# Optimization experiments

Measured on AMD Instinct MI355X. Metric: run time of the kernel, lower is better.

Reference implementation:

```python
import jax, jax.numpy as jnp
import numpy as np

B, T, D, H = 2, 2048, 1024, 16
DK = D // H


def setup_inputs() -> dict:
    key = jax.random.key(0)
    ks = jax.random.split(key, 12)
    s = 0.02
    return {
        "query": jax.random.normal(ks[0], (B, T, D), jnp.float32),
        "key": jax.random.normal(ks[1], (B, T, D), jnp.float32),
        "value": jax.random.normal(ks[2], (B, T, D), jnp.float32),
        "mask": jax.random.randint(ks[3], (B, T), 0, 2) != 0,  # True = keep
        "Wq": jax.random.normal(ks[4], (D, D), jnp.float32) * s,
        "bq": jnp.zeros((D,), jnp.float32),
        "Wk": jax.random.normal(ks[5], (D, D), jnp.float32) * s,
        "bk": jnp.zeros((D,), jnp.float32),
        "Wv": jax.random.normal(ks[6], (D, D), jnp.float32) * s,
        "bv": jnp.zeros((D,), jnp.float32),
        "Wo": jax.random.normal(ks[7], (D, D), jnp.float32) * s,
        "bo": jnp.zeros((D,), jnp.float32),
    }


def _split_heads(x):
    # [B, S, D] -> [B, H, S, DK]
    b, s, _ = x.shape
    return x.reshape(b, s, H, DK).transpose(0, 2, 1, 3)


def reference(query, key, value, mask, Wq, bq, Wk, bk, Wv, bv, Wo, bo):
    # torch Linear: y = x @ W.T + b
    q = _split_heads(query @ Wq.T + bq)   # [B,H,T,DK]
    k = _split_heads(key @ Wk.T + bk)     # [B,H,S,DK]
    v = _split_heads(value @ Wv.T + bv)   # [B,H,S,DK]
    scale = 1.0 / np.sqrt(DK).astype(np.float32)
    scores = jnp.einsum('bhtd,bhsd->bhts', q, k) * scale  # [B,H,T,S]
    # key-padding mask [B,S] -> broadcast [B,1,1,S], True = keep
    scores = jnp.where(mask[:, None, None, :], scores, -jnp.inf)
    attn = jax.nn.softmax(scores, axis=-1)
    out = jnp.einsum('bhts,bhsd->bhtd', attn, v)           # [B,H,T,DK]
    out = out.transpose(0, 2, 1, 3).reshape(query.shape[0], -1, D)
    return out @ Wo.T + bo
```

## Files before the change

kernel.cpp:

```cpp
#include <hip/hip_runtime.h>
#include <stdint.h>

#define B_SZ 2
#define T_SEQ 2048
#define DMODEL 1024
#define NHEAD 16
#define DKH 64
#define M_ROWS (B_SZ * T_SEQ)

#define LDT 72

#define INP_E  4194304u
#define W_E    1048576u

typedef __bf16 bf16x8 __attribute__((ext_vector_type(8)));
typedef float  f32x4  __attribute__((ext_vector_type(4)));

__device__ __forceinline__ unsigned short f2bf(float f) {
    unsigned u = __builtin_bit_cast(unsigned, f);
    u += 0x7fffu + ((u >> 16) & 1u);
    return (unsigned short)(u >> 16);
}
__device__ __forceinline__ uint4 cvt8(const float* p) {
    float4 f0 = *(const float4*)p, f1 = *(const float4*)(p + 4);
    uint4 r;
    r.x = (unsigned)f2bf(f0.x) | ((unsigned)f2bf(f0.y) << 16);
    r.y = (unsigned)f2bf(f0.z) | ((unsigned)f2bf(f0.w) << 16);
    r.z = (unsigned)f2bf(f1.x) | ((unsigned)f2bf(f1.y) << 16);
    r.w = (unsigned)f2bf(f1.z) | ((unsigned)f2bf(f1.w) << 16);
    return r;
}

__device__ __forceinline__ void async16(const unsigned short* g, unsigned short* l) {
    __builtin_amdgcn_global_load_lds(
        (const __attribute__((address_space(1))) void*)g,
        (__attribute__((address_space(3))) void*)l, 16, 0, 0);
}

__global__ __launch_bounds__(256) void cvt_all(
    const float* __restrict__ q, const float* __restrict__ k, const float* __restrict__ v,
    const float* __restrict__ wq, const float* __restrict__ wk,
    const float* __restrict__ wv, const float* __restrict__ wo,
    unsigned short* __restrict__ wsb)
{
    int blk = blockIdx.x;
    const float* src; unsigned short* dst; int lb;
    if      (blk < 2048) { src = q;  dst = wsb;                       lb = blk; }
    else if (blk < 4096) { src = k;  dst = wsb + INP_E;               lb = blk - 2048; }
    else if (blk < 6144) { src = v;  dst = wsb + 2 * INP_E;           lb = blk - 4096; }
    else if (blk < 6656) { src = wq; dst = wsb + 3 * INP_E;           lb = blk - 6144; }
    else if (blk < 7168) { src = wk; dst = wsb + 3 * INP_E + W_E;     lb = blk - 6656; }
    else if (blk < 7680) { src = wv; dst = wsb + 3 * INP_E + 2 * W_E; lb = blk - 7168; }
    else                 { src = wo; dst = wsb + 3 * INP_E + 3 * W_E; lb = blk - 7680; }
    size_t i = ((size_t)lb * 256 + threadIdx.x) * 8;
    *(uint4*)&dst[i] = cvt8(src + i);
}

template<int C_MODE, int MT>
__device__ __forceinline__ void gemm_core(
    const unsigned short* __restrict__ A, const unsigned short* __restrict__ W,
    const float* __restrict__ bias, void* __restrict__ C,
    int N, int K, int bx, int by,
    unsigned short* sA, unsigned short* sB)
{
    const int tid  = threadIdx.x;
    const int wave = tid >> 6, lane = tid & 63;
    const int quad = lane >> 4, l15 = lane & 15;
    const int TM = MT * 32;
    const int m0 = by * TM, n0 = bx * 128;
    const int wm = (wave & 1) * (MT * 16), wn = (wave >> 1) * 64;

    f32x4 acc[MT][4] = {};

    for (int k0 = 0; k0 < K; k0 += 64) {
        __syncthreads();
        #pragma unroll
        for (int i = 0; i < MT; i++) {
            int c   = tid + 256 * i;
            int row = c >> 3;
            int gk  = ((c & 7) ^ (row & 7)) * 8;
            int sb  = (wave * 64 + 256 * i) * 8;
            async16(&A[(size_t)(m0 + row) * K + k0 + gk], sA + sb);
        }
        #pragma unroll
        for (int i = 0; i < 4; i++) {
            int c   = tid + 256 * i;
            int row = c >> 3;
            int gk  = ((c & 7) ^ (row & 7)) * 8;
            int sb  = (wave * 64 + 256 * i) * 8;
            async16(&W[(size_t)(n0 + row) * K + k0 + gk], sB + sb);
        }
        __syncthreads();
        const int sw = l15 & 7;
        #pragma unroll
        for (int ks = 0; ks < 2; ks++) {
            bf16x8 af[MT], bfv[4];
            #pragma unroll
            for (int mt = 0; mt < MT; mt++)
                af[mt] = *(const bf16x8*)&sA[(wm + mt * 16 + l15) * 64 +
                                             (((ks * 4 + quad) ^ sw) * 8)];
            #pragma unroll
            for (int nt = 0; nt < 4; nt++)
                bfv[nt] = *(const bf16x8*)&sB[(wn + nt * 16 + l15) * 64 +
                                              (((ks * 4 + quad) ^ sw) * 8)];
            #pragma unroll
            for (int mt = 0; mt < MT; mt++)
                #pragma unroll
                for (int nt = 0; nt < 4; nt++)
                    acc[mt][nt] = __builtin_amdgcn_mfma_f32_16x16x32_bf16(
                        af[mt], bfv[nt], acc[mt][nt], 0, 0, 0);
        }
    }

    if (C_MODE == 2) {
        #pragma unroll
        for (int mt = 0; mt < MT; mt++) {
            #pragma unroll
            for (int r = 0; r < 4; r++) {
                int m = m0 + wm + mt * 16 + quad * 4 + r;
                float bm = bias[m];
                #pragma unroll
                for (int nt = 0; nt < 4; nt++) {
                    int n = n0 + wn + nt * 16 + l15;
                    int bb = n >> 11, t = n & 2047;
                    ((unsigned short*)C)[((size_t)bb * 1024 + m) * 2048 + t] =
                        f2bf(acc[mt][nt][r] + bm);
                }
            }
        }
    } else {
        #pragma unroll
        for (int nt = 0; nt < 4; nt++) {
            int n = n0 + wn + nt * 16 + l15;
            float bv = bias[n];
            #pragma unroll
            for (int mt = 0; mt < MT; mt++) {
                #pragma unroll
                for (int r = 0; r < 4; r++) {
                    int m = m0 + wm + mt * 16 + quad * 4 + r;
                    float val = acc[mt][nt][r] + bv;
                    if (C_MODE == 1) ((float*)C)[(size_t)m * N + n] = val;
                    else ((unsigned short*)C)[(size_t)m * N + n] = f2bf(val);
                }
            }
        }
    }
}

__global__ __launch_bounds__(256) void gemm_qkv(
    const unsigned short* __restrict__ Qb, const unsigned short* __restrict__ Kb,
    const unsigned short* __restrict__ Vb,
    const unsigned short* __restrict__ Wqb, const unsigned short* __restrict__ Wkb,
    const unsigned short* __restrict__ Wvb,
    const float* __restrict__ bq, const float* __restrict__ bk, const float* __restrict__ bv,
    unsigned short* __restrict__ Qp, unsigned short* __restrict__ Kp,
    unsigned short* __restrict__ Vt)
{
    __shared__ __align__(16) unsigned short sA[128 * 64];
    __shared__ __align__(16) unsigned short sB[128 * 64];
    const int z = blockIdx.z, id = blockIdx.x;
    if (z < 2) {
        gemm_core<0, 4>(z ? Kb : Qb, z ? Wkb : Wqb, z ? bk : bq, z ? Kp : Qp,
                        DMODEL, DMODEL, id & 7, id >> 3, sA, sB);
    } else {
        gemm_core<2, 4>(Wvb, Vb, bv, Vt, M_ROWS, DMODEL, id & 31, id >> 5, sA, sB);
    }
}

__global__ __launch_bounds__(256) void gemm_o(
    const unsigned short* __restrict__ AO, const unsigned short* __restrict__ Wob,
    const float* __restrict__ bo, float* __restrict__ out)
{
    __shared__ __align__(16) unsigned short sA[64 * 64];
    __shared__ __align__(16) unsigned short sB[128 * 64];
    const int id = blockIdx.x;
    gemm_core<1, 2>(AO, Wob, bo, out, DMODEL, DMODEL, id & 7, id >> 3, sA, sB);
}

#define QBLK 128
#define KVB 64

__global__ __launch_bounds__(512, 4) void attn_kernel(
    const unsigned short* __restrict__ Qp,
    const unsigned short* __restrict__ Kp,
    const unsigned short* __restrict__ Vt,
    const int* __restrict__ maskp,
    unsigned short* __restrict__ Op)
{
    __shared__ __align__(16) unsigned short sKV[2][2][KVB * 64];
    __shared__ __align__(16) unsigned short sP[8 * 32 * LDT];
    __shared__ float smf[T_SEQ];

    const int tid  = threadIdx.x;
    const int wave = tid >> 6, lane = tid & 63;
    const int g    = wave >> 2, wl = wave & 3;
    const int quad = lane >> 4, l15 = lane & 15;
    const int qblk = blockIdx.x, h = blockIdx.y, b = blockIdx.z;

    const float SCL2 = 0.125f * 1.44269504089f;
    const float MNEG = -30000.f;

    bf16x8 aq[2][2];
    #pragma unroll
    for (int mt = 0; mt < 2; mt++) {
        const int qrow = qblk * QBLK + wl * 32 + mt * 16 + l15;
        const unsigned short* qptr =
            Qp + (size_t)(b * T_SEQ + qrow) * DMODEL + h * DKH + quad * 8;
        aq[mt][0] = *(const bf16x8*)qptr;
        aq[mt][1] = *(const bf16x8*)(qptr + 32);
    }

    const unsigned short* Kb_ = Kp + (size_t)b * T_SEQ * DMODEL + h * DKH;
    const unsigned short* VtB = Vt + ((size_t)b * DMODEL + h * DKH) * T_SEQ;

    f32x4 O[2][4] = {};
    float l_r[2][4] = {};
    unsigned short* sPw = sP + wave * 32 * LDT;

    #pragma unroll
    for (int j = 0; j < 4; j++) {
        int i = tid + 512 * j;
        smf[i] = maskp[b * T_SEQ + i] ? 0.f : MNEG;
    }

    const int sw = l15 & 7;
    for (int rr = 0; rr < T_SEQ / (2 * KVB); ++rr) {
        #pragma unroll
        for (int i = 0; i < 2; i++) {
            int c    = tid + 512 * i;
            int tile = c >> 9, cc = c & 511;
            int row  = cc >> 3;
            int gk   = ((cc & 7) ^ (row & 7)) * 8;
            int sb   = (wave * 64 + 512 * i) * 8;
            int key0 = rr * 128 + tile * 64;
            async16(&Kb_[(size_t)(key0 + row) * DMODEL + gk], &sKV[0][0][0] + sb);
            async16(&VtB[(size_t)row * T_SEQ + key0 + gk], &sKV[1][0][0] + sb);
        }
        __syncthreads();

        const unsigned short* sKp = &sKV[0][g][0];
        const unsigned short* sVp = &sKV[1][g][0];
        const int s0 = (2 * rr + g) * KVB;

        f32x4 S[2][4];
        __builtin_amdgcn_s_setprio(1);
        #pragma unroll
        for (int nt = 0; nt < 4; nt++) {
            const unsigned short* kr = &sKp[(nt * 16 + l15) * 64];
            const bf16x8 kf0 = *(const bf16x8*)&kr[(quad ^ sw) * 8];
            const bf16x8 kf1 = *(const bf16x8*)&kr[((quad + 4) ^ sw) * 8];
            #pragma unroll
            for (int mt = 0; mt < 2; mt++) {
                f32x4 z = {};
                z = __builtin_amdgcn_mfma_f32_16x16x32_bf16(aq[mt][0], kf0, z, 0, 0, 0);
                z = __builtin_amdgcn_mfma_f32_16x16x32_bf16(aq[mt][1], kf1, z, 0, 0, 0);
                S[mt][nt] = z;
            }
        }
        __builtin_amdgcn_s_setprio(0);

        #pragma unroll
        for (int mt = 0; mt < 2; mt++) {
            #pragma unroll
            for (int nt = 0; nt < 4; nt++) {
                float madd = smf[s0 + nt * 16 + l15];
                #pragma unroll
                for (int r = 0; r < 4; r++) {
                    float p = __builtin_amdgcn_exp2f(fmaf(S[mt][nt][r], SCL2, madd));
                    l_r[mt][r] += p;
                    unsigned u = __builtin_bit_cast(unsigned, p) + 0x8000u;
                    sPw[(mt * 16 + quad * 4 + r) * LDT + nt * 16 + l15] =
                        (unsigned short)(u >> 16);
                }
            }
        }

        bf16x8 ap0[2], ap1[2];
        #pragma unroll
        for (int mt = 0; mt < 2; mt++) {
            ap0[mt] = *(const bf16x8*)&sPw[(mt * 16 + l15) * LDT + quad * 8];
            ap1[mt] = *(const bf16x8*)&sPw[(mt * 16 + l15) * LDT + 32 + quad * 8];
        }
        __builtin_amdgcn_s_setprio(1);
        #pragma unroll
        for (int nt = 0; nt < 4; nt++) {
            const unsigned short* vr = &sVp[(nt * 16 + l15) * 64];
            const bf16x8 vf0 = *(const bf16x8*)&vr[(quad ^ sw) * 8];
            const bf16x8 vf1 = *(const bf16x8*)&vr[((quad + 4) ^ sw) * 8];
            #pragma unroll
            for (int mt = 0; mt < 2; mt++) {
                O[mt][nt] = __builtin_amdgcn_mfma_f32_16x16x32_bf16(
                    ap0[mt], vf0, O[mt][nt], 0, 0, 0);
                O[mt][nt] = __builtin_amdgcn_mfma_f32_16x16x32_bf16(
                    ap1[mt], vf1, O[mt][nt], 0, 0, 0);
            }
        }
        __builtin_amdgcn_s_setprio(0);

        __syncthreads();
    }

    #pragma unroll
    for (int mt = 0; mt < 2; mt++) {
        #pragma unroll
        for (int r = 0; r < 4; r++) {
            float l = l_r[mt][r];
            l += __shfl_xor(l, 1);
            l += __shfl_xor(l, 2);
            l += __shfl_xor(l, 4);
            l += __shfl_xor(l, 8);
            l_r[mt][r] = l;
        }
    }

    float* OM = (float*)&sKV[0][0][0];
    float* LM = (float*)sP;
    if (g == 1) {
        #pragma unroll
        for (int mt = 0; mt < 2; mt++) {
            #pragma unroll
            for (int r = 0; r < 4; r++) {
                int row = wl * 32 + mt * 16 + quad * 4 + r;
                if (l15 == 0) LM[row] = l_r[mt][r];
                #pragma unroll
                for (int nt = 0; nt < 4; nt++)
                    OM[row * 64 + nt * 16 + l15] = O[mt][nt][r];
            }
        }
    }
    __syncthreads();
    if (g == 0) {
        #pragma unroll
        for (int mt = 0; mt < 2; mt++) {
            #pragma unroll
            for (int r = 0; r < 4; r++) {
                int row = wl * 32 + mt * 16 + quad * 4 + r;
                float inv = 1.0f / fmaxf(l_r[mt][r] + LM[row], 1e-30f);
                int q = qblk * QBLK + row;
                #pragma unroll
                for (int nt = 0; nt < 4; nt++) {
                    float val = (O[mt][nt][r] + OM[row * 64 + nt * 16 + l15]) * inv;
                    Op[(size_t)(b * T_SEQ + q) * DMODEL + h * DKH + nt * 16 + l15] =
                        f2bf(val);
                }
            }
        }
    }
}

template<int A_BF16, int W_BF16, int C_MODE>
__global__ __launch_bounds__(256) void gemm_bt_cvt(
    const void* __restrict__ A_, const void* __restrict__ W_,
    const float* __restrict__ bias, void* __restrict__ C_,
    int M, int N, int K)
{
    __shared__ __align__(16) unsigned short sA[128 * LDT];
    __shared__ __align__(16) unsigned short sB[128 * LDT];
    const int tid  = threadIdx.x;
    const int wave = tid >> 6, lane = tid & 63;
    const int quad = lane >> 4, l15 = lane & 15;
    const int m0 = blockIdx.y * 128, n0 = blockIdx.x * 128;
    const int wm = (wave & 1) * 64, wn = (wave >> 1) * 64;
    f32x4 acc[4][4] = {};
    for (int k0 = 0; k0 < K; k0 += 64) {
        __syncthreads();
        #pragma unroll
        for (int i = 0; i < 4; i++) {
            int c = tid + 256 * i;
            int row = c >> 3, koff = (c & 7) * 8;
            if (A_BF16)
                *(uint4*)&sA[row * LDT + koff] =
                    *(const uint4*)&((const unsigned short*)A_)[(size_t)(m0 + row) * K + k0 + koff];
            else
                *(uint4*)&sA[row * LDT + koff] =
                    cvt8((const float*)A_ + (size_t)(m0 + row) * K + k0 + koff);
            if (W_BF16)
                *(uint4*)&sB[row * LDT + koff] =
                    *(const uint4*)&((const unsigned short*)W_)[(size_t)(n0 + row) * K + k0 + koff];
            else
                *(uint4*)&sB[row * LDT + koff] =
                    cvt8((const float*)W_ + (size_t)(n0 + row) * K + k0 + koff);
        }
        __syncthreads();
        #pragma unroll
        for (int ks = 0; ks < 2; ks++) {
            bf16x8 af[4], bfr[4];
            #pragma unroll
            for (int mt = 0; mt < 4; mt++)
                af[mt] = *(const bf16x8*)&sA[(wm + mt * 16 + l15) * LDT + ks * 32 + quad * 8];
            #pragma unroll
            for (int nt = 0; nt < 4; nt++)
                bfr[nt] = *(const bf16x8*)&sB[(wn + nt * 16 + l15) * LDT + ks * 32 + quad * 8];
            #pragma unroll
            for (int mt = 0; mt < 4; mt++)
                #pragma unroll
                for (int nt = 0; nt < 4; nt++)
                    acc[mt][nt] = __builtin_amdgcn_mfma_f32_16x16x32_bf16(
                        af[mt], bfr[nt], acc[mt][nt], 0, 0, 0);
        }
    }
    if (C_MODE == 2) {
        #pragma unroll
        for (int mt = 0; mt < 4; mt++)
            #pragma unroll
            for (int r = 0; r < 4; r++) {
                int m = m0 + wm + mt * 16 + quad * 4 + r;
                float bm = bias[m];
                #pragma unroll
                for (int nt = 0; nt < 4; nt++) {
                    int n = n0 + wn + nt * 16 + l15;
                    int bb = n >> 11, t = n & 2047;
                    ((unsigned short*)C_)[((size_t)bb * 1024 + m) * 2048 + t] =
                        f2bf(acc[mt][nt][r] + bm);
                }
            }
    } else {
        #pragma unroll
        for (int nt = 0; nt < 4; nt++) {
            int n = n0 + wn + nt * 16 + l15;
            float bv = bias[n];
            #pragma unroll
            for (int mt = 0; mt < 4; mt++)
                #pragma unroll
                for (int r = 0; r < 4; r++) {
                    int m = m0 + wm + mt * 16 + quad * 4 + r;
                    float val = acc[mt][nt][r] + bv;
                    if (C_MODE == 1) ((float*)C_)[(size_t)m * N + n] = val;
                    else ((unsigned short*)C_)[(size_t)m * N + n] = f2bf(val);
                }
        }
    }
}

extern "C" void kernel_launch(void* const* d_in, const int* in_sizes, int n_in,
                              void* d_out, int out_size, void* d_ws, size_t ws_size,
                              hipStream_t stream)
{
    const float* q  = (const float*)d_in[0];
    const float* k  = (const float*)d_in[1];
    const float* v  = (const float*)d_in[2];
    const int*   mk = (const int*)d_in[3];
    const float* Wq = (const float*)d_in[4];
    const float* bq = (const float*)d_in[5];
    const float* Wk = (const float*)d_in[6];
    const float* bk = (const float*)d_in[7];
    const float* Wv = (const float*)d_in[8];
    const float* bv = (const float*)d_in[9];
    const float* Wo = (const float*)d_in[10];
    const float* bo = (const float*)d_in[11];
    float* out = (float*)d_out;

    unsigned short* wsb = (unsigned short*)d_ws;
    const dim3 gA(T_SEQ / QBLK, NHEAD, B_SZ);

    if (ws_size >= (size_t)64 * 1024 * 1024) {
        unsigned short* Qb  = wsb;
        unsigned short* Kb  = wsb + INP_E;
        unsigned short* Vb  = wsb + 2 * INP_E;
        unsigned short* Wqb = wsb + 3 * INP_E;
        unsigned short* Wkb = wsb + 3 * INP_E + W_E;
        unsigned short* Wvb = wsb + 3 * INP_E + 2 * W_E;
        unsigned short* Wob = wsb + 3 * INP_E + 3 * W_E;
        unsigned short* Qp  = wsb + 4 * INP_E;
        unsigned short* Kp  = wsb + 5 * INP_E;
        unsigned short* Vt  = wsb + 6 * INP_E;
        unsigned short* AO  = wsb + 7 * INP_E;

        cvt_all<<<8192, 256, 0, stream>>>(q, k, v, Wq, Wk, Wv, Wo, wsb);
        gemm_qkv<<<dim3(256, 1, 3), 256, 0, stream>>>(
            Qb, Kb, Vb, Wqb, Wkb, Wvb, bq, bk, bv, Qp, Kp, Vt);
        attn_kernel<<<gA, 512, 0, stream>>>(Qp, Kp, Vt, mk, AO);
        gemm_o<<<dim3(512, 1, 1), 256, 0, stream>>>(AO, Wob, bo, out);
    } else {
        unsigned short* Qp = wsb;
        unsigned short* Kp = wsb + INP_E;
        unsigned short* Vt = wsb + 2 * INP_E;
        unsigned short* AO = wsb + 3 * INP_E;
        const dim3 gN(DMODEL / 128, M_ROWS / 128);
        const dim3 gV(M_ROWS / 128, DMODEL / 128);
        gemm_bt_cvt<0, 0, 0><<<gN, 256, 0, stream>>>(q, Wq, bq, Qp, M_ROWS, DMODEL, DMODEL);
        gemm_bt_cvt<0, 0, 0><<<gN, 256, 0, stream>>>(k, Wk, bk, Kp, M_ROWS, DMODEL, DMODEL);
        gemm_bt_cvt<0, 0, 2><<<gV, 256, 0, stream>>>(Wv, v, bv, Vt, DMODEL, M_ROWS, DMODEL);
        attn_kernel<<<gA, 512, 0, stream>>>(Qp, Kp, Vt, mk, AO);
        gemm_bt_cvt<1, 0, 1><<<gN, 256, 0, stream>>>(AO, Wo, bo, out, M_ROWS, DMODEL, DMODEL);
    }
}
```

Baseline: 231.9 us.

## Compute transposed attention scores to keep P in registers, skip LDS round-trip

Swaps MFMA operand order so the score tile comes out transposed (keys along rows), which lets each lane pack its softmax probabilities directly into the bf16x8 B-operand of the PV MFMA instead of writing P to shared memory and reading it back. To make this line up, V tiles are now loaded with 4-byte async global-to-LDS copies into a permuted layout computed once before the loop. The row-sum reduction and the epilogue are reworked for the new layout, with padded stride and vectorized output stores. This removes the per-iteration P shared-memory traffic and shrinks LDS use, at the cost of four times as many, smaller V load instructions.

```diff
diff --git a/kernel.cpp b/kernel.cpp
--- a/kernel.cpp
+++ b/kernel.cpp
@@ -35,6 +35,11 @@
     __builtin_amdgcn_global_load_lds(
         (const __attribute__((address_space(1))) void*)g,
         (__attribute__((address_space(3))) void*)l, 16, 0, 0);
+}
+__device__ __forceinline__ void async4(const unsigned short* g, unsigned short* l) {
+    __builtin_amdgcn_global_load_lds(
+        (const __attribute__((address_space(1))) void*)g,
+        (__attribute__((address_space(3))) void*)l, 4, 0, 0);
 }
 
 __global__ __launch_bounds__(256) void cvt_all(
@@ -187,9 +192,10 @@
     const int* __restrict__ maskp,
     unsigned short* __restrict__ Op)
 {
-    __shared__ __align__(16) unsigned short sKV[2][2][KVB * 64];
-    __shared__ __align__(16) unsigned short sP[8 * 32 * LDT];
-    __shared__ float smf[T_SEQ];
+    __shared__ __align__(16) unsigned char sMEM[40960];
+    unsigned short* sK  = (unsigned short*)sMEM;
+    unsigned short* sV  = (unsigned short*)(sMEM + 16384);
+    float*          smf = (float*)(sMEM + 32768);
 
     const int tid  = threadIdx.x;
     const int wave = tid >> 6, lane = tid & 63;
@@ -213,9 +219,37 @@
     const unsigned short* Kb_ = Kp + (size_t)b * T_SEQ * DMODEL + h * DKH;
     const unsigned short* VtB = Vt + ((size_t)b * DMODEL + h * DKH) * T_SEQ;
 
+    int kOff[2], kSb[2];
+    #pragma unroll
+    for (int i = 0; i < 2; i++) {
+        int c = tid + 512 * i;
+        int tile = c >> 9, cc = c & 511;
+        int row = cc >> 3;
+        int gk = ((cc & 7) ^ (row & 7)) * 8;
+        kOff[i] = (tile * 64 + row) * DMODEL + gk;
+        kSb[i]  = (wave * 64 + 512 * i) * 8;
+    }
+    int vOff[8], vSb[8];
+    #pragma unroll
+    for (int i = 0; i < 8; i++) {
+        int P    = wave * 2048 + i * 256 + lane * 4;
+        int tile = P >> 13;
+        int rp   = P & 8191;
+        int row  = rp >> 7;
+        int cb   = (rp >> 4) & 7;
+        int slot = (rp >> 2) & 3;
+        int c    = cb ^ (row & 7);
+        int f    = c * 4 + slot;
+        int g2   = ((f >> 4) << 1) | ((f >> 1) & 1);
+        int qq   = (f >> 2) & 3;
+        int r2   = (f & 1) * 2;
+        int keyoff = g2 * 16 + qq * 4 + r2;
+        vOff[i] = row * T_SEQ + tile * 64 + keyoff;
+        vSb[i]  = (wave * 2048 + i * 256) >> 1;
+    }
+
     f32x4 O[2][4] = {};
-    float l_r[2][4] = {};
-    unsigned short* sPw = sP + wave * 32 * LDT;
+    float l_r[2] = {0.f, 0.f};
 
     #pragma unroll
     for (int j = 0; j < 4; j++) {
@@ -226,61 +260,50 @@
     const int sw = l15 & 7;
     for (int rr = 0; rr < T_SEQ / (2 * KVB); ++rr) {
         #pragma unroll
-        for (int i = 0; i < 2; i++) {
-            int c    = tid + 512 * i;
-            int tile = c >> 9, cc = c & 511;
-            int row  = cc >> 3;
-            int gk   = ((cc & 7) ^ (row & 7)) * 8;
-            int sb   = (wave * 64 + 512 * i) * 8;
-            int key0 = rr * 128 + tile * 64;
-            async16(&Kb_[(size_t)(key0 + row) * DMODEL + gk], &sKV[0][0][0] + sb);
-            async16(&VtB[(size_t)row * T_SEQ + key0 + gk], &sKV[1][0][0] + sb);
-        }
+        for (int i = 0; i < 2; i++)
+            async16(&Kb_[(size_t)rr * 128 * DMODEL + kOff[i]], sK + kSb[i]);
+        #pragma unroll
+        for (int i = 0; i < 8; i++)
+            async4(&VtB[(size_t)rr * 128 + vOff[i]], sV + vSb[i]);
         __syncthreads();
 
-        const unsigned short* sKp = &sKV[0][g][0];
-        const unsigned short* sVp = &sKV[1][g][0];
+        const unsigned short* sKp = sK + g * 4096;
+        const unsigned short* sVp = sV + g * 4096;
         const int s0 = (2 * rr + g) * KVB;
 
-        f32x4 S[2][4];
+        f32x4 ST[2][4];
         __builtin_amdgcn_s_setprio(1);
         #pragma unroll
-        for (int nt = 0; nt < 4; nt++) {
-            const unsigned short* kr = &sKp[(nt * 16 + l15) * 64];
+        for (int kt = 0; kt < 4; kt++) {
+            const unsigned short* kr = &sKp[(kt * 16 + l15) * 64];
             const bf16x8 kf0 = *(const bf16x8*)&kr[(quad ^ sw) * 8];
             const bf16x8 kf1 = *(const bf16x8*)&kr[((quad + 4) ^ sw) * 8];
             #pragma unroll
             for (int mt = 0; mt < 2; mt++) {
                 f32x4 z = {};
-                z = __builtin_amdgcn_mfma_f32_16x16x32_bf16(aq[mt][0], kf0, z, 0, 0, 0);
-                z = __builtin_amdgcn_mfma_f32_16x16x32_bf16(aq[mt][1], kf1, z, 0, 0, 0);
-                S[mt][nt] = z;
+                z = __builtin_amdgcn_mfma_f32_16x16x32_bf16(kf0, aq[mt][0], z, 0, 0, 0);
+                z = __builtin_amdgcn_mfma_f32_16x16x32_bf16(kf1, aq[mt][1], z, 0, 0, 0);
+                ST[mt][kt] = z;
             }
         }
         __builtin_amdgcn_s_setprio(0);
 
-        #pragma unroll
-        for (int mt = 0; mt < 2; mt++) {
-            #pragma unroll
-            for (int nt = 0; nt < 4; nt++) {
-                float madd = smf[s0 + nt * 16 + l15];
+        bf16x8 pb[2][2];
+        #pragma unroll
+        for (int kt = 0; kt < 4; kt++) {
+            float4 m4 = *(const float4*)&smf[s0 + kt * 16 + quad * 4];
+            float ma[4] = {m4.x, m4.y, m4.z, m4.w};
+            #pragma unroll
+            for (int mt = 0; mt < 2; mt++) {
                 #pragma unroll
                 for (int r = 0; r < 4; r++) {
-                    float p = __builtin_amdgcn_exp2f(fmaf(S[mt][nt][r], SCL2, madd));
-                    l_r[mt][r] += p;
-                    unsigned u = __builtin_bit_cast(unsigned, p) + 0x8000u;
-                    sPw[(mt * 16 + quad * 4 + r) * LDT + nt * 16 + l15] =
-                        (unsigned short)(u >> 16);
+                    float p = __builtin_amdgcn_exp2f(fmaf(ST[mt][kt][r], SCL2, ma[r]));
+                    l_r[mt] += p;
+                    pb[mt][kt >> 1][(kt & 1) * 4 + r] = (__bf16)p;
                 }
             }
         }
 
-        bf16x8 ap0[2], ap1[2];
-        #pragma unroll
-        for (int mt = 0; mt < 2; mt++) {
-            ap0[mt] = *(const bf16x8*)&sPw[(mt * 16 + l15) * LDT + quad * 8];
-            ap1[mt] = *(const bf16x8*)&sPw[(mt * 16 + l15) * LDT + 32 + quad * 8];
-        }
         __builtin_amdgcn_s_setprio(1);
         #pragma unroll
         for (int nt = 0; nt < 4; nt++) {
@@ -290,9 +313,9 @@
             #pragma unroll
             for (int mt = 0; mt < 2; mt++) {
                 O[mt][nt] = __builtin_amdgcn_mfma_f32_16x16x32_bf16(
-                    ap0[mt], vf0, O[mt][nt], 0, 0, 0);
+                    vf0, pb[mt][0], O[mt][nt], 0, 0, 0);
                 O[mt][nt] = __builtin_amdgcn_mfma_f32_16x16x32_bf16(
-                    ap1[mt], vf1, O[mt][nt], 0, 0, 0);
+                    vf1, pb[mt][1], O[mt][nt], 0, 0, 0);
             }
         }
         __builtin_amdgcn_s_setprio(0);
@@ -302,47 +325,42 @@
 
     #pragma unroll
     for (int mt = 0; mt < 2; mt++) {
-        #pragma unroll
-        for (int r = 0; r < 4; r++) {
-            float l = l_r[mt][r];
-            l += __shfl_xor(l, 1);
-            l += __shfl_xor(l, 2);
-            l += __shfl_xor(l, 4);
-            l += __shfl_xor(l, 8);
-            l_r[mt][r] = l;
-        }
-    }
-
-    float* OM = (float*)&sKV[0][0][0];
-    float* LM = (float*)sP;
+        float l = l_r[mt];
+        l += __shfl_xor(l, 16);
+        l += __shfl_xor(l, 32);
+        l_r[mt] = l;
+    }
+
+    float* OM = (float*)sMEM;
+    float* LM = (float*)(sMEM + 33280);
     if (g == 1) {
         #pragma unroll
         for (int mt = 0; mt < 2; mt++) {
-            #pragma unroll
-            for (int r = 0; r < 4; r++) {
-                int row = wl * 32 + mt * 16 + quad * 4 + r;
-                if (l15 == 0) LM[row] = l_r[mt][r];
-                #pragma unroll
-                for (int nt = 0; nt < 4; nt++)
-                    OM[row * 64 + nt * 16 + l15] = O[mt][nt][r];
-            }
+            int row = wl * 32 + mt * 16 + l15;
+            if (quad == 0) LM[row] = l_r[mt];
+            #pragma unroll
+            for (int nt = 0; nt < 4; nt++)
+                #pragma unroll
+                for (int r = 0; r < 4; r++)
+                    OM[row * 65 + nt * 16 + quad * 4 + r] = O[mt][nt][r];
         }
     }
     __syncthreads();
     if (g == 0) {
         #pragma unroll
         for (int mt = 0; mt < 2; mt++) {
-            #pragma unroll
-            for (int r = 0; r < 4; r++) {
-                int row = wl * 32 + mt * 16 + quad * 4 + r;
-                float inv = 1.0f / fmaxf(l_r[mt][r] + LM[row], 1e-30f);
-                int q = qblk * QBLK + row;
-                #pragma unroll
-                for (int nt = 0; nt < 4; nt++) {
-                    float val = (O[mt][nt][r] + OM[row * 64 + nt * 16 + l15]) * inv;
-                    Op[(size_t)(b * T_SEQ + q) * DMODEL + h * DKH + nt * 16 + l15] =
-                        f2bf(val);
-                }
+            int row = wl * 32 + mt * 16 + l15;
+            float inv = 1.0f / fmaxf(l_r[mt] + LM[row], 1e-30f);
+            int qg = qblk * QBLK + row;
+            unsigned short* op = Op + (size_t)(b * T_SEQ + qg) * DMODEL + h * DKH;
+            #pragma unroll
+            for (int nt = 0; nt < 4; nt++) {
+                ushort4 w;
+                w.x = f2bf((O[mt][nt][0] + OM[row * 65 + nt * 16 + quad * 4 + 0]) * inv);
+                w.y = f2bf((O[mt][nt][1] + OM[row * 65 + nt * 16 + quad * 4 + 1]) * inv);
+                w.z = f2bf((O[mt][nt][2] + OM[row * 65 + nt * 16 + quad * 4 + 2]) * inv);
+                w.w = f2bf((O[mt][nt][3] + OM[row * 65 + nt * 16 + quad * 4 + 3]) * inv);
+                *(ushort4*)&op[nt * 16 + quad * 4] = w;
             }
         }
     }
```

After: 224.9 us. -3.0%, faster.
